# Optimization experiments

Hardware: AMD Instinct MI355X
Metric: run time of the kernel (lower is better)

## Reference

```python
import jax, jax.numpy as jnp
import numpy as np


def setup_inputs() -> dict:
    key = jax.random.key(0)
    B, N, F = 32, 8192, 256
    x = jax.random.normal(key, (B, N, F), dtype=jnp.float32)
    return {"x": x, "k": 1024}


def reference(x, k):
    # Sort rows of each graph by last feature, descending, keep top k.
    # Original: per-batch argsort(desc) + gather, then truncate to k (N > k here).
    # lax.top_k returns indices of the k largest values in descending order,
    # equivalent to argsort(desc)[:k] without a full sort.
    _, idx = jax.lax.top_k(x[..., -1], k)          # idx: [B, k]
    out = jnp.take_along_axis(x, idx[:, :, None], axis=1)  # [B, k, F]
    return out
```

## Files before the change

### kernel.cpp

```cpp
#include <hip/hip_runtime.h>
#include <hip/hip_bf16.h>

#define B_DIM 32
#define N_DIM 8192
#define F_DIM 256
#define K_DIM 1024
#define RUNS_PER_B 8
#define RUN_LEN 1024

__device__ __forceinline__ unsigned int f32_ord(float v) {
    unsigned int u = __float_as_uint(v);
    return (u & 0x80000000u) ? ~u : (u | 0x80000000u);
}

__global__ __launch_bounds__(256)
void sort_runs_kernel(const float* __restrict__ x,
                      unsigned long long* __restrict__ runs) {
    __shared__ unsigned long long keys[RUN_LEN];

    const int blk = blockIdx.x;
    const int b   = blk >> 3;
    const int c   = blk & 7;
    const float* xb = x + (size_t)b * N_DIM * F_DIM;
    const int base = c * RUN_LEN;

    for (int i = threadIdx.x; i < RUN_LEN; i += 256) {
        int row = base + i;
        float v = xb[(size_t)row * F_DIM + (F_DIM - 1)];
        keys[i] = ((unsigned long long)f32_ord(v) << 32) |
                  (unsigned int)(N_DIM - 1 - row);
    }
    __syncthreads();

    for (unsigned int kk = 2; kk <= RUN_LEN; kk <<= 1) {
        for (unsigned int jj = kk >> 1; jj > 0; jj >>= 1) {
            for (unsigned int p = threadIdx.x; p < RUN_LEN / 2; p += 256) {
                unsigned int i = ((p & ~(jj - 1)) << 1) | (p & (jj - 1));
                unsigned int j = i | jj;
                unsigned long long a  = keys[i];
                unsigned long long bb = keys[j];
                bool desc = ((i & kk) == 0);
                if (desc ? (a < bb) : (a > bb)) {
                    keys[i] = bb;
                    keys[j] = a;
                }
            }
            __syncthreads();
        }
    }

    unsigned long long* r = runs + (size_t)blk * RUN_LEN;
    for (int i = threadIdx.x; i < RUN_LEN; i += 256) r[i] = keys[i];
}

__global__ __launch_bounds__(256)
void merge_topk_kernel(const unsigned long long* __restrict__ runs,
                       int* __restrict__ idx_out) {
    __shared__ unsigned long long A[K_DIM];
    __shared__ unsigned long long Bv[K_DIM];

    const int b = blockIdx.x;
    const unsigned long long* rb = runs + (size_t)b * N_DIM;

    for (int i = threadIdx.x; i < K_DIM; i += 256) A[i] = rb[i];

    for (int r = 1; r < RUNS_PER_B; ++r) {
        for (int i = threadIdx.x; i < K_DIM; i += 256) Bv[i] = rb[r * K_DIM + i];
        __syncthreads();

        for (int i = threadIdx.x; i < K_DIM; i += 256) {
            unsigned long long m = Bv[K_DIM - 1 - i];
            if (m > A[i]) A[i] = m;
        }
        __syncthreads();

        for (unsigned int jj = K_DIM / 2; jj > 0; jj >>= 1) {
            for (unsigned int p = threadIdx.x; p < K_DIM / 2; p += 256) {
                unsigned int i = ((p & ~(jj - 1)) << 1) | (p & (jj - 1));
                unsigned int j = i | jj;
                unsigned long long a  = A[i];
                unsigned long long cc = A[j];
                if (a < cc) { A[i] = cc; A[j] = a; }
            }
            __syncthreads();
        }
    }

    for (int i = threadIdx.x; i < K_DIM; i += 256) {
        unsigned int low = (unsigned int)(A[i] & 0xFFFFFFFFu);
        idx_out[b * K_DIM + i] = (int)(N_DIM - 1 - low);
    }
}

__global__ __launch_bounds__(256)
void gather_rows_kernel(const float* __restrict__ x,
                        const int* __restrict__ idx,
                        float* __restrict__ out) {
    size_t gid = (size_t)blockIdx.x * blockDim.x + threadIdx.x;
    int f4     = (int)(gid & (F_DIM / 4 - 1));
    size_t row = gid >> 6;
    int b      = (int)(row >> 10);
    int src    = idx[row];

    const float4* src_ptr =
        (const float4*)(x + ((size_t)b * N_DIM + (size_t)src) * F_DIM) + f4;
    ((float4*)out)[gid] = *src_ptr;
}

extern "C" void kernel_launch(void* const* d_in, const int* in_sizes, int n_in,
                              void* d_out, int out_size, void* d_ws, size_t ws_size,
                              hipStream_t stream) {
    const float* x = (const float*)d_in[0];
    float* out = (float*)d_out;

    unsigned long long* runs = (unsigned long long*)d_ws;
    int* idx_ws = (int*)((char*)d_ws + (size_t)B_DIM * N_DIM * 8);

    sort_runs_kernel<<<B_DIM * RUNS_PER_B, 256, 0, stream>>>(x, runs);
    merge_topk_kernel<<<B_DIM, 256, 0, stream>>>(runs, idx_ws);

    const size_t total_f4 = (size_t)B_DIM * K_DIM * F_DIM / 4;
    gather_rows_kernel<<<(int)(total_f4 / 256), 256, 0, stream>>>(x, idx_ws, out);
}
```

Baseline: 370.9 us.

## Parallelize top-k merge as a tree reduction and widen sort blocks

The run-sorting kernel now uses 512 threads so each bitonic step is a single compare-exchange per thread, and it writes results back with vectorized 16-byte stores. The merge kernel loads all eight sorted runs into shared memory and merges them in a three-level tree, with each level's pairwise max and bitonic cleanup running in parallel across 1024 threads. This replaces seven sequential merge rounds done by 256 threads. The cost is 64KB of shared memory per merge block, and only 32 blocks are launched.

```diff
diff --git a/kernel.cpp b/kernel.cpp
--- a/kernel.cpp
+++ b/kernel.cpp
@@ -6,88 +6,89 @@
 #define F_DIM 256
 #define K_DIM 1024
 #define RUNS_PER_B 8
-#define RUN_LEN 1024
 
 __device__ __forceinline__ unsigned int f32_ord(float v) {
     unsigned int u = __float_as_uint(v);
     return (u & 0x80000000u) ? ~u : (u | 0x80000000u);
 }
 
-__global__ __launch_bounds__(256)
+__global__ __launch_bounds__(512)
 void sort_runs_kernel(const float* __restrict__ x,
                       unsigned long long* __restrict__ runs) {
-    __shared__ unsigned long long keys[RUN_LEN];
+    __shared__ unsigned long long K[K_DIM];
 
     const int blk = blockIdx.x;
     const int b   = blk >> 3;
     const int c   = blk & 7;
-    const float* xb = x + (size_t)b * N_DIM * F_DIM;
-    const int base = c * RUN_LEN;
+    const float* xcol = x + (size_t)b * N_DIM * F_DIM + (F_DIM - 1);
+    const int base = c * K_DIM;
 
-    for (int i = threadIdx.x; i < RUN_LEN; i += 256) {
+    for (int i = threadIdx.x; i < K_DIM; i += 512) {
         int row = base + i;
-        float v = xb[(size_t)row * F_DIM + (F_DIM - 1)];
-        keys[i] = ((unsigned long long)f32_ord(v) << 32) |
-                  (unsigned int)(N_DIM - 1 - row);
+        float v = xcol[(size_t)row * F_DIM];
+        K[i] = ((unsigned long long)f32_ord(v) << 32) |
+               (unsigned int)(N_DIM - 1 - row);
     }
     __syncthreads();
 
-    for (unsigned int kk = 2; kk <= RUN_LEN; kk <<= 1) {
+    for (unsigned int kk = 2; kk <= K_DIM; kk <<= 1) {
         for (unsigned int jj = kk >> 1; jj > 0; jj >>= 1) {
-            for (unsigned int p = threadIdx.x; p < RUN_LEN / 2; p += 256) {
-                unsigned int i = ((p & ~(jj - 1)) << 1) | (p & (jj - 1));
+            unsigned int p = threadIdx.x;
+            unsigned int i = ((p & ~(jj - 1)) << 1) | (p & (jj - 1));
+            unsigned int j = i | jj;
+            unsigned long long a  = K[i];
+            unsigned long long bb = K[j];
+            bool desc = ((i & kk) == 0);
+            if (desc ? (a < bb) : (a > bb)) { K[i] = bb; K[j] = a; }
+            __syncthreads();
+        }
+    }
+
+    ulonglong2* dst = (ulonglong2*)(runs + (size_t)blk * K_DIM);
+    const ulonglong2* src = (const ulonglong2*)K;
+    dst[threadIdx.x] = src[threadIdx.x];
+}
+
+__global__ __launch_bounds__(1024)
+void merge_topk_kernel(const unsigned long long* __restrict__ runs,
+                       int* __restrict__ idx_out) {
+    __shared__ unsigned long long K[N_DIM];
+
+    const int b = blockIdx.x;
+    const ulonglong2* src = (const ulonglong2*)(runs + (size_t)b * N_DIM);
+    ulonglong2* Kv = (ulonglong2*)K;
+    for (unsigned int i = threadIdx.x; i < N_DIM / 2; i += 1024) Kv[i] = src[i];
+    __syncthreads();
+
+    for (int level = 0; level < 3; ++level) {
+        const unsigned int m      = 4u >> level;
+        const unsigned int stride = 1024u << level;
+        const unsigned int shift  = 11 + level;
+
+        for (unsigned int t = threadIdx.x; t < m * 1024u; t += 1024) {
+            unsigned int g = t >> 10, i = t & 1023u;
+            unsigned int a = g << shift;
+            unsigned long long bv = K[a + stride + 1023u - i];
+            if (bv > K[a + i]) K[a + i] = bv;
+        }
+        __syncthreads();
+
+        for (unsigned int jj = 512; jj > 0; jj >>= 1) {
+            for (unsigned int t = threadIdx.x; t < m * 512u; t += 1024) {
+                unsigned int g = t >> 9, p = t & 511u;
+                unsigned int base = g << shift;
+                unsigned int i = base + (((p & ~(jj - 1)) << 1) | (p & (jj - 1)));
                 unsigned int j = i | jj;
-                unsigned long long a  = keys[i];
-                unsigned long long bb = keys[j];
-                bool desc = ((i & kk) == 0);
-                if (desc ? (a < bb) : (a > bb)) {
-                    keys[i] = bb;
-                    keys[j] = a;
-                }
+                unsigned long long a = K[i];
+                unsigned long long c = K[j];
+                if (a < c) { K[i] = c; K[j] = a; }
             }
             __syncthreads();
         }
     }
 
-    unsigned long long* r = runs + (size_t)blk * RUN_LEN;
-    for (int i = threadIdx.x; i < RUN_LEN; i += 256) r[i] = keys[i];
-}
-
-__global__ __launch_bounds__(256)
-void merge_topk_kernel(const unsigned long long* __restrict__ runs,
-                       int* __restrict__ idx_out) {
-    __shared__ unsigned long long A[K_DIM];
-    __shared__ unsigned long long Bv[K_DIM];
-
-    const int b = blockIdx.x;
-    const unsigned long long* rb = runs + (size_t)b * N_DIM;
-
-    for (int i = threadIdx.x; i < K_DIM; i += 256) A[i] = rb[i];
-
-    for (int r = 1; r < RUNS_PER_B; ++r) {
-        for (int i = threadIdx.x; i < K_DIM; i += 256) Bv[i] = rb[r * K_DIM + i];
-        __syncthreads();
-
-        for (int i = threadIdx.x; i < K_DIM; i += 256) {
-            unsigned long long m = Bv[K_DIM - 1 - i];
-            if (m > A[i]) A[i] = m;
-        }
-        __syncthreads();
-
-        for (unsigned int jj = K_DIM / 2; jj > 0; jj >>= 1) {
-            for (unsigned int p = threadIdx.x; p < K_DIM / 2; p += 256) {
-                unsigned int i = ((p & ~(jj - 1)) << 1) | (p & (jj - 1));
-                unsigned int j = i | jj;
-                unsigned long long a  = A[i];
-                unsigned long long cc = A[j];
-                if (a < cc) { A[i] = cc; A[j] = a; }
-            }
-            __syncthreads();
-        }
-    }
-
-    for (int i = threadIdx.x; i < K_DIM; i += 256) {
-        unsigned int low = (unsigned int)(A[i] & 0xFFFFFFFFu);
+    for (unsigned int i = threadIdx.x; i < K_DIM; i += 1024) {
+        unsigned int low = (unsigned int)(K[i] & 0xFFFFFFFFu);
         idx_out[b * K_DIM + i] = (int)(N_DIM - 1 - low);
     }
 }
@@ -116,8 +117,8 @@
     unsigned long long* runs = (unsigned long long*)d_ws;
     int* idx_ws = (int*)((char*)d_ws + (size_t)B_DIM * N_DIM * 8);
 
-    sort_runs_kernel<<<B_DIM * RUNS_PER_B, 256, 0, stream>>>(x, runs);
-    merge_topk_kernel<<<B_DIM, 256, 0, stream>>>(runs, idx_ws);
+    sort_runs_kernel<<<B_DIM * RUNS_PER_B, 512, 0, stream>>>(x, runs);
+    merge_topk_kernel<<<B_DIM, 1024, 0, stream>>>(runs, idx_ws);
 
     const size_t total_f4 = (size_t)B_DIM * K_DIM * F_DIM / 4;
     gather_rows_kernel<<<(int)(total_f4 / 256), 256, 0, stream>>>(x, idx_ws, out);
```

After: 343.5 us. -7.4%, faster.
